# Optimization experiments

Hardware: AMD Instinct MI355X
Metric: run time of the kernel (lower is better)

The kernel has to match this reference:

```python
import jax, jax.numpy as jnp
import numpy as np

B, N = 4, 2048
PARAM_G = 0.125       # recovery rate
VIRUS_DEATH = 8e-5    # disease-induced death rate


def setup_inputs() -> dict:
    key = jax.random.key(0)
    ks = jax.random.split(key, 7)
    return {
        "param_b": jax.random.uniform(ks[0], (B, N, 1), jnp.float32),
        "contact": jax.random.uniform(ks[1], (B, N, 1), jnp.float32),
        "mob": jax.random.uniform(ks[2], (B, N, N), jnp.float32),
        "SIR": jax.random.uniform(ks[3], (B, N, 4), jnp.float32),
        "sps": jax.random.uniform(ks[4], (B, N, N), jnp.float32),
        # original loads birth_china.npy / death_china.npy and divides by 365000
        "nature_birth": jax.random.uniform(ks[5], (N, 1), jnp.float32) / 365000.0,
        "nature_death": jax.random.uniform(ks[6], (N, 1), jnp.float32) / 365000.0,
    }


def reference(param_b, contact, mob, SIR, sps, nature_birth, nature_death):
    b, n = SIR.shape[0], SIR.shape[1]
    eye = jnp.eye(n, dtype=bool)
    # zero out diagonal (no self-mobility)
    F_nm = jnp.where(eye[None], 0.0, mob)            # [B,N,N]
    sps_m = jnp.where(eye[None], 0.0, sps)           # [B,N,N]
    # torch: P = F_nm / F_nm.sum(1).unsqueeze(2)  -> divide row i,col j by sum_k F[b,k,j] broadcast over last dim
    col_sum = F_nm.sum(axis=1)                       # [B,N]
    P = F_nm / col_sum[:, :, None]                   # [B,N,N]
    fai = F_nm.sum(axis=(1, 2))[:, None]             # [B,1]

    S = SIR[..., 0:1]
    I = SIR[..., 1:2]
    R = SIR[..., 2:3]
    I_sum = SIR[..., 3:4]
    pop = S + I + R                                  # [B,N,1]
    tau = pop.sum(axis=1)                            # [B,1]
    m = (fai / tau)[:, :, None]                      # [B,1,1] mobility rate (scalar per batch)

    birth = nature_birth[None]                       # [1,N,1]
    death = nature_death[None]                       # [1,N,1]

    I_new = S / pop * param_b * contact * I          # new infections

    # flux term: sum_j m * X[b,j] * P[b,i,j] == m * (P @ X), fused matvec instead of [B,N,N] broadcast
    flux = lambda X: m * jnp.matmul(P, X)            # [B,N,1]

    R_t = R + PARAM_G * I - death * R - m * R + flux(R)
    I_t = I + I_new - death * I - PARAM_G * I - VIRUS_DEATH * I - m * I + flux(I)
    S_t = S - I_new - death * S + birth * pop - m * S + flux(S)
    I_sum_t = I_sum + I_new

    R0 = param_b * contact / (death + PARAM_G + VIRUS_DEATH + m)
    W_arrive = param_b * contact - death - PARAM_G - VIRUS_DEATH

    Ht_SIR = jnp.concatenate([R0, I_new, S_t, I_t, R_t, I_sum_t], axis=-1)       # [B,N,6]
    arrive1 = jnp.concatenate(
        [W_arrive, jnp.broadcast_to(m, S.shape), I, pop], axis=-1)               # [B,N,4]
    arrive2 = jnp.stack([sps_m, P], axis=-1)                                     # [B,N,N,2]
    return Ht_SIR, arrive1, arrive2
```

## Files before the change

### kernel.cpp

```cpp
#include <hip/hip_runtime.h>

#define NN 2048
#define BB 4
#define PARAM_G 0.125f
#define VIRUS_DEATH 8e-5f

#define WS_ROWS 8192
#define WS_ROWI 16384
#define WS_ROWR 24576
#define WS_FAI  32768
#define WS_TAU  32772

__global__ __launch_bounds__(256) void k_colsum(const float* __restrict__ mob,
                                                float* ws) {
    int t  = threadIdx.x;
    int i0 = blockIdx.x * 64;
    int j  = blockIdx.y * 1024 + t * 4;
    int b  = blockIdx.z;
    const float* base = mob + ((size_t)b * NN + i0) * NN + j;
    float4 acc = make_float4(0.f, 0.f, 0.f, 0.f);
    for (int r = 0; r < 64; ++r) {
        float4 v = *(const float4*)(base + (size_t)r * NN);
        unsigned d = (unsigned)((i0 + r) - j);
        if (d < 4u) ((float*)&v)[d] = 0.0f;
        acc.x += v.x; acc.y += v.y; acc.z += v.z; acc.w += v.w;
    }
    atomicAdd(&ws[b * NN + j + 0], acc.x);
    atomicAdd(&ws[b * NN + j + 1], acc.y);
    atomicAdd(&ws[b * NN + j + 2], acc.z);
    atomicAdd(&ws[b * NN + j + 3], acc.w);
}

__global__ __launch_bounds__(256) void k_scalars(const float* __restrict__ SIR,
                                                 float* ws) {
    int b = blockIdx.x;
    int t = threadIdx.x;
    float accT = 0.f, accF = 0.f;
    for (int n = t; n < NN; n += 256) {
        float4 s = *(const float4*)(SIR + ((size_t)b * NN + n) * 4);
        accT += s.x + s.y + s.z;
        accF += ws[b * NN + n];
    }
    for (int off = 32; off; off >>= 1) {
        accT += __shfl_down(accT, off);
        accF += __shfl_down(accF, off);
    }
    __shared__ float red[2][4];
    int w = t >> 6, lane = t & 63;
    if (lane == 0) { red[0][w] = accT; red[1][w] = accF; }
    __syncthreads();
    if (t == 0) {
        ws[WS_TAU + b] = red[0][0] + red[0][1] + red[0][2] + red[0][3];
        ws[WS_FAI + b] = red[1][0] + red[1][1] + red[1][2] + red[1][3];
    }
}

__global__ __launch_bounds__(256) void k_main(const float* __restrict__ mob,
                                              const float* __restrict__ sps,
                                              const float* __restrict__ SIR,
                                              float* ws,
                                              float* __restrict__ out2) {
    __shared__ __align__(16) float sS[NN];
    __shared__ __align__(16) float sI[NN];
    __shared__ __align__(16) float sR[NN];
    int t = threadIdx.x;
    int b = blockIdx.y;
    for (int j = t; j < NN; j += 256) {
        float4 s = *(const float4*)(SIR + ((size_t)b * NN + j) * 4);
        sS[j] = s.x; sI[j] = s.y; sR[j] = s.z;
    }
    __syncthreads();

    int w = t >> 6, lane = t & 63;
    int i = blockIdx.x * 4 + w;
    float invc = 1.0f / ws[b * NN + i];
    size_t rowoff = ((size_t)b * NN + i) * NN;
    const float* mrow = mob + rowoff;
    const float* srow = sps + rowoff;
    float* orow = out2 + rowoff * 2;

    float aS = 0.f, aI = 0.f, aR = 0.f;
    #pragma unroll
    for (int iter = 0; iter < 8; ++iter) {
        int j = iter * 256 + lane * 4;
        float4 mv = *(const float4*)(mrow + j);
        float4 sv = *(const float4*)(srow + j);
        unsigned d = (unsigned)(i - j);
        if (d < 4u) { ((float*)&mv)[d] = 0.0f; ((float*)&sv)[d] = 0.0f; }
        float4 xS = *(const float4*)&sS[j];
        float4 xI = *(const float4*)&sI[j];
        float4 xR = *(const float4*)&sR[j];
        aS += mv.x * xS.x + mv.y * xS.y + mv.z * xS.z + mv.w * xS.w;
        aI += mv.x * xI.x + mv.y * xI.y + mv.z * xI.z + mv.w * xI.w;
        aR += mv.x * xR.x + mv.y * xR.y + mv.z * xR.z + mv.w * xR.w;
        float4 o0 = make_float4(sv.x, mv.x * invc, sv.y, mv.y * invc);
        float4 o1 = make_float4(sv.z, mv.z * invc, sv.w, mv.w * invc);
        *(float4*)(orow + (size_t)j * 2)     = o0;
        *(float4*)(orow + (size_t)j * 2 + 4) = o1;
    }
    for (int off = 32; off; off >>= 1) {
        aS += __shfl_down(aS, off);
        aI += __shfl_down(aI, off);
        aR += __shfl_down(aR, off);
    }
    if (lane == 0) {
        ws[WS_ROWS + b * NN + i] = aS;
        ws[WS_ROWI + b * NN + i] = aI;
        ws[WS_ROWR + b * NN + i] = aR;
    }
}

__global__ __launch_bounds__(256) void k_epi(const float* __restrict__ param_b,
                                             const float* __restrict__ contact,
                                             const float* __restrict__ SIR,
                                             const float* __restrict__ nb,
                                             const float* __restrict__ nd,
                                             const float* ws,
                                             float* __restrict__ out0,
                                             float* __restrict__ out1) {
    int g = blockIdx.x * 256 + threadIdx.x;
    int b = g >> 11;
    int n = g & (NN - 1);
    float4 sir = *(const float4*)(SIR + (size_t)g * 4);
    float S = sir.x, I = sir.y, R = sir.z, Isum = sir.w;
    float pb = param_b[g], ct = contact[g];
    float birth = nb[n], death = nd[n];
    float cs = ws[g];
    float rS = ws[WS_ROWS + g], rI = ws[WS_ROWI + g], rR = ws[WS_ROWR + g];
    float m = ws[WS_FAI + b] / ws[WS_TAU + b];

    float pop   = S + I + R;
    float pbc   = pb * ct;
    float I_new = S / pop * pbc * I;
    float icv   = 1.0f / cs;
    float fS = m * rS * icv, fI = m * rI * icv, fR = m * rR * icv;

    float R_t    = R + PARAM_G * I - death * R - m * R + fR;
    float I_t    = I + I_new - death * I - PARAM_G * I - VIRUS_DEATH * I - m * I + fI;
    float S_t    = S - I_new - death * S + birth * pop - m * S + fS;
    float Isum_t = Isum + I_new;
    float R0     = pbc / (death + PARAM_G + VIRUS_DEATH + m);
    float W      = pbc - death - PARAM_G - VIRUS_DEATH;

    float* o0 = out0 + (size_t)g * 6;
    *(float2*)(o0 + 0) = make_float2(R0, I_new);
    *(float2*)(o0 + 2) = make_float2(S_t, I_t);
    *(float2*)(o0 + 4) = make_float2(R_t, Isum_t);
    *(float4*)(out1 + (size_t)g * 4) = make_float4(W, m, I, pop);
}

extern "C" void kernel_launch(void* const* d_in, const int* in_sizes, int n_in,
                              void* d_out, int out_size, void* d_ws, size_t ws_size,
                              hipStream_t stream) {
    const float* param_b = (const float*)d_in[0];
    const float* contact = (const float*)d_in[1];
    const float* mob     = (const float*)d_in[2];
    const float* SIR     = (const float*)d_in[3];
    const float* sps     = (const float*)d_in[4];
    const float* nb      = (const float*)d_in[5];
    const float* nd      = (const float*)d_in[6];

    float* out  = (float*)d_out;
    float* out0 = out;
    float* out1 = out + (size_t)BB * NN * 6;
    float* out2 = out1 + (size_t)BB * NN * 4;
    float* ws   = (float*)d_ws;

    hipMemsetAsync(ws, 0, (size_t)BB * NN * sizeof(float), stream);

    k_colsum <<<dim3(32, 2, BB),  256, 0, stream>>>(mob, ws);
    k_scalars<<<BB,               256, 0, stream>>>(SIR, ws);
    k_main   <<<dim3(NN / 4, BB), 256, 0, stream>>>(mob, sps, SIR, ws, out2);
    k_epi    <<<(BB * NN) / 256,  256, 0, stream>>>(param_b, contact, SIR, nb, nd,
                                                    ws, out0, out1);
}
```

Measured before the change: 333.2 us.

## Rebalance reduction kernels and process two rows per block in main pass

The column-sum kernel now uses twice as many blocks, each covering 32 rows, and folds the per-batch total (fai) into it through wave reductions and atomics. The separate scalar kernel becomes a 16-block tau reduction that also accumulates with atomics, so the workspace memset is widened to cover both scalars. The main kernel has each wave handle two rows with float2 loads and one float4 interleaved store per iteration, so the shared SIR staging is amortised over twice as many rows. The intent is more parallelism in the small reduction kernels and less per-block staging overhead, at the cost of narrower loads and extra atomics.

```diff
diff --git a/kernel.cpp b/kernel.cpp
--- a/kernel.cpp
+++ b/kernel.cpp
@@ -10,16 +10,18 @@
 #define WS_ROWR 24576
 #define WS_FAI  32768
 #define WS_TAU  32772
+#define WS_ZERO_FLOATS (WS_TAU + BB)
 
 __global__ __launch_bounds__(256) void k_colsum(const float* __restrict__ mob,
                                                 float* ws) {
     int t  = threadIdx.x;
-    int i0 = blockIdx.x * 64;
+    int i0 = blockIdx.x * 32;
     int j  = blockIdx.y * 1024 + t * 4;
     int b  = blockIdx.z;
     const float* base = mob + ((size_t)b * NN + i0) * NN + j;
     float4 acc = make_float4(0.f, 0.f, 0.f, 0.f);
-    for (int r = 0; r < 64; ++r) {
+    #pragma unroll 8
+    for (int r = 0; r < 32; ++r) {
         float4 v = *(const float4*)(base + (size_t)r * NN);
         unsigned d = (unsigned)((i0 + r) - j);
         if (d < 4u) ((float*)&v)[d] = 0.0f;
@@ -29,30 +31,29 @@
     atomicAdd(&ws[b * NN + j + 1], acc.y);
     atomicAdd(&ws[b * NN + j + 2], acc.z);
     atomicAdd(&ws[b * NN + j + 3], acc.w);
+    float s = acc.x + acc.y + acc.z + acc.w;
+    for (int off = 32; off; off >>= 1) s += __shfl_down(s, off);
+    if ((t & 63) == 0) atomicAdd(&ws[WS_FAI + b], s);
 }
 
-__global__ __launch_bounds__(256) void k_scalars(const float* __restrict__ SIR,
-                                                 float* ws) {
-    int b = blockIdx.x;
-    int t = threadIdx.x;
-    float accT = 0.f, accF = 0.f;
-    for (int n = t; n < NN; n += 256) {
+__global__ __launch_bounds__(256) void k_tau(const float* __restrict__ SIR,
+                                             float* ws) {
+    int b  = blockIdx.x >> 2;
+    int n0 = (blockIdx.x & 3) * 512;
+    int t  = threadIdx.x;
+    float acc = 0.f;
+    #pragma unroll
+    for (int k = 0; k < 2; ++k) {
+        int n = n0 + k * 256 + t;
         float4 s = *(const float4*)(SIR + ((size_t)b * NN + n) * 4);
-        accT += s.x + s.y + s.z;
-        accF += ws[b * NN + n];
+        acc += s.x + s.y + s.z;
     }
-    for (int off = 32; off; off >>= 1) {
-        accT += __shfl_down(accT, off);
-        accF += __shfl_down(accF, off);
-    }
-    __shared__ float red[2][4];
-    int w = t >> 6, lane = t & 63;
-    if (lane == 0) { red[0][w] = accT; red[1][w] = accF; }
+    for (int off = 32; off; off >>= 1) acc += __shfl_down(acc, off);
+    __shared__ float red[4];
+    int w = t >> 6;
+    if ((t & 63) == 0) red[w] = acc;
     __syncthreads();
-    if (t == 0) {
-        ws[WS_TAU + b] = red[0][0] + red[0][1] + red[0][2] + red[0][3];
-        ws[WS_FAI + b] = red[1][0] + red[1][1] + red[1][2] + red[1][3];
-    }
+    if (t == 0) atomicAdd(&ws[WS_TAU + b], red[0] + red[1] + red[2] + red[3]);
 }
 
 __global__ __launch_bounds__(256) void k_main(const float* __restrict__ mob,
@@ -72,41 +73,43 @@
     __syncthreads();
 
     int w = t >> 6, lane = t & 63;
-    int i = blockIdx.x * 4 + w;
-    float invc = 1.0f / ws[b * NN + i];
-    size_t rowoff = ((size_t)b * NN + i) * NN;
-    const float* mrow = mob + rowoff;
-    const float* srow = sps + rowoff;
-    float* orow = out2 + rowoff * 2;
-
-    float aS = 0.f, aI = 0.f, aR = 0.f;
+    int i0 = blockIdx.x * 8;
     #pragma unroll
-    for (int iter = 0; iter < 8; ++iter) {
-        int j = iter * 256 + lane * 4;
-        float4 mv = *(const float4*)(mrow + j);
-        float4 sv = *(const float4*)(srow + j);
-        unsigned d = (unsigned)(i - j);
-        if (d < 4u) { ((float*)&mv)[d] = 0.0f; ((float*)&sv)[d] = 0.0f; }
-        float4 xS = *(const float4*)&sS[j];
-        float4 xI = *(const float4*)&sI[j];
-        float4 xR = *(const float4*)&sR[j];
-        aS += mv.x * xS.x + mv.y * xS.y + mv.z * xS.z + mv.w * xS.w;
-        aI += mv.x * xI.x + mv.y * xI.y + mv.z * xI.z + mv.w * xI.w;
-        aR += mv.x * xR.x + mv.y * xR.y + mv.z * xR.z + mv.w * xR.w;
-        float4 o0 = make_float4(sv.x, mv.x * invc, sv.y, mv.y * invc);
-        float4 o1 = make_float4(sv.z, mv.z * invc, sv.w, mv.w * invc);
-        *(float4*)(orow + (size_t)j * 2)     = o0;
-        *(float4*)(orow + (size_t)j * 2 + 4) = o1;
-    }
-    for (int off = 32; off; off >>= 1) {
-        aS += __shfl_down(aS, off);
-        aI += __shfl_down(aI, off);
-        aR += __shfl_down(aR, off);
-    }
-    if (lane == 0) {
-        ws[WS_ROWS + b * NN + i] = aS;
-        ws[WS_ROWI + b * NN + i] = aI;
-        ws[WS_ROWR + b * NN + i] = aR;
+    for (int k = 0; k < 2; ++k) {
+        int i = i0 + w + 4 * k;
+        float invc = 1.0f / ws[b * NN + i];
+        size_t rowoff = ((size_t)b * NN + i) * NN;
+        const float* mrow = mob + rowoff;
+        const float* srow = sps + rowoff;
+        float* orow = out2 + rowoff * 2;
+        float aS = 0.f, aI = 0.f, aR = 0.f;
+        #pragma unroll 4
+        for (int iter = 0; iter < 16; ++iter) {
+            int j2 = iter * 128 + lane * 2;
+            float2 mv = *(const float2*)(mrow + j2);
+            float2 sv = *(const float2*)(srow + j2);
+            unsigned d = (unsigned)(i - j2);
+            if (d == 0u)      { mv.x = 0.f; sv.x = 0.f; }
+            else if (d == 1u) { mv.y = 0.f; sv.y = 0.f; }
+            float2 xS = *(const float2*)&sS[j2];
+            float2 xI = *(const float2*)&sI[j2];
+            float2 xR = *(const float2*)&sR[j2];
+            aS += mv.x * xS.x + mv.y * xS.y;
+            aI += mv.x * xI.x + mv.y * xI.y;
+            aR += mv.x * xR.x + mv.y * xR.y;
+            *(float4*)(orow + (size_t)j2 * 2) =
+                make_float4(sv.x, mv.x * invc, sv.y, mv.y * invc);
+        }
+        for (int off = 32; off; off >>= 1) {
+            aS += __shfl_down(aS, off);
+            aI += __shfl_down(aI, off);
+            aR += __shfl_down(aR, off);
+        }
+        if (lane == 0) {
+            ws[WS_ROWS + b * NN + i] = aS;
+            ws[WS_ROWI + b * NN + i] = aI;
+            ws[WS_ROWR + b * NN + i] = aR;
+        }
     }
 }
 
@@ -166,11 +169,11 @@
     float* out2 = out1 + (size_t)BB * NN * 4;
     float* ws   = (float*)d_ws;
 
-    hipMemsetAsync(ws, 0, (size_t)BB * NN * sizeof(float), stream);
+    hipMemsetAsync(ws, 0, (size_t)WS_ZERO_FLOATS * sizeof(float), stream);
 
-    k_colsum <<<dim3(32, 2, BB),  256, 0, stream>>>(mob, ws);
-    k_scalars<<<BB,               256, 0, stream>>>(SIR, ws);
-    k_main   <<<dim3(NN / 4, BB), 256, 0, stream>>>(mob, sps, SIR, ws, out2);
-    k_epi    <<<(BB * NN) / 256,  256, 0, stream>>>(param_b, contact, SIR, nb, nd,
-                                                    ws, out0, out1);
+    k_colsum<<<dim3(64, 2, BB),  256, 0, stream>>>(mob, ws);
+    k_tau   <<<16,               256, 0, stream>>>(SIR, ws);
+    k_main  <<<dim3(NN / 8, BB), 256, 0, stream>>>(mob, sps, SIR, ws, out2);
+    k_epi   <<<(BB * NN) / 256,  256, 0, stream>>>(param_b, contact, SIR, nb, nd,
+                                                   ws, out0, out1);
 }
```

After: 295.1 us. -11.4%, faster.
